# Kernel optimization log

Hardware: AMD Instinct MI355X
Metric: run time of the kernel (lower is better)

Reference implementation:

```python
import jax, jax.numpy as jnp
import numpy as np

HEAD_DIM = 64
EPS = 1e-06


def yat_dense(x, kernel, bias):
    # YatDense (nmn): y = (x.W)^2 / (||x - w||^2 + eps) * alpha_scale + b
    dot = x @ kernel                                  # [..., F]
    x_sq = jnp.sum(x * x, axis=-1, keepdims=True)     # [..., 1]
    w_sq = jnp.sum(kernel * kernel, axis=0)           # [F]
    dist = x_sq + w_sq - 2.0 * dot                    # squared euclidean distance
    y = (dot * dot) / (dist + EPS)
    feats = kernel.shape[1]
    scale = np.sqrt(feats) / np.log1p(feats)          # alpha=1 scaling
    return y * jnp.asarray(scale, x.dtype) + bias


def apply_rope(q, k):
    # q,k: [B,H,T,D]; interleaved-pair rotation, base 10000 (dim=HEAD_DIM)
    B, H, T, D = q.shape
    half = D // 2
    pos = jnp.arange(T, dtype=jnp.float32)
    freqs = 10000.0 ** (-jnp.arange(half, dtype=jnp.float32) / half)
    ang = pos[:, None] * freqs[None, :]               # [T, half]
    sin = jnp.sin(ang)[None, None, :, :, None]        # [1,1,T,half,1]
    cos = jnp.cos(ang)[None, None, :, :, None]

    def rot(t):
        ts = t.reshape(B, H, T, half, 2)
        t0, t1 = ts[..., 0:1], ts[..., 1:2]
        out = jnp.concatenate([t0 * cos - t1 * sin, t1 * cos + t0 * sin], axis=-1)
        return out.reshape(B, H, T, D)

    return rot(q), rot(k)


def setup_inputs() -> dict:
    key = jax.random.key(0)
    B, T, C, H = 2, 2048, 1024, 16
    k1, k2, k3, k4, k5 = jax.random.split(key, 5)
    x = jax.random.normal(k1, (B, T, C), dtype=jnp.float32)
    # causal mask, broadcast over batch
    mask = jnp.broadcast_to(jnp.tril(jnp.ones((T, T), dtype=bool))[None], (B, T, T))
    s = 1.0 / np.sqrt(C)
    w_attn = jax.random.normal(k2, (C, 3 * C), dtype=jnp.float32) * s
    b_attn = jnp.zeros((3 * C,), dtype=jnp.float32)
    w_proj = jax.random.normal(k3, (C, C), dtype=jnp.float32) * s
    b_proj = jnp.zeros((C,), dtype=jnp.float32)
    return {"x": x, "mask": mask, "w_attn": w_attn, "b_attn": b_attn,
            "w_proj": w_proj, "b_proj": b_proj}


def reference(x, mask, w_attn, b_attn, w_proj, b_proj):
    B, T, C = x.shape
    H = C // HEAD_DIM
    qkv = yat_dense(x, w_attn, b_attn)                     # [B,T,3C]
    qkv = qkv.reshape(B, T, 3, H, HEAD_DIM)
    q, k, v = jnp.moveaxis(qkv, 2, 0)                      # each [B,T,H,hd]
    q = jnp.swapaxes(q, 1, 2)                              # [B,H,T,hd]
    k = jnp.swapaxes(k, 1, 2)
    v = jnp.swapaxes(v, 1, 2)
    q, k = apply_rope(q, k)
    scale = jnp.asarray(np.sqrt(HEAD_DIM), x.dtype)
    attn = jnp.einsum('bhqd,bhkd->bhqk', q, k) / scale     # [B,H,T,T]
    neg = jnp.finfo(x.dtype).min
    attn = jnp.where(mask[:, None, :, :], attn, neg)
    attn = jax.nn.softmax(attn, axis=-1)
    out = jnp.einsum('bhqk,bhkd->bhqd', attn, v)           # [B,H,T,hd]
    out = jnp.swapaxes(out, 1, 2).reshape(B, T, C)
    return yat_dense(out, w_proj, b_proj)
```

## Files before the change

kernel.cpp:

```cpp
#include <hip/hip_runtime.h>
#include <hip/hip_bf16.h>
#include <cmath>

#define BB 2
#define TT 2048
#define CC 1024
#define HH 16
#define DD 64
#define ROWS (BB*TT)
#define N1 (3*CC)
#define EPS 1e-6f

using short8 = __attribute__((ext_vector_type(8))) short;
using f32x4  = __attribute__((ext_vector_type(4))) float;

__device__ __forceinline__ void gl_lds16(const __hip_bfloat16* g, unsigned short* l) {
    __builtin_amdgcn_global_load_lds(
        (const __attribute__((address_space(1))) unsigned int*)(g),
        (__attribute__((address_space(3))) unsigned int*)(l), 16, 0, 0);
}

__device__ __forceinline__ unsigned int bf16pair(float a, float b) {
    __hip_bfloat16 ha = (__hip_bfloat16)a, hb = (__hip_bfloat16)b;
    unsigned short ua = *(unsigned short*)&ha, ub = *(unsigned short*)&hb;
    return (unsigned int)ua | ((unsigned int)ub << 16);
}

__device__ __forceinline__ float bf2f(unsigned short u) {
    unsigned int v = (unsigned int)u << 16;
    return *(float*)&v;
}

__global__ void aux_rowsq(const float* __restrict__ X, float* __restrict__ xsq,
                          __hip_bfloat16* __restrict__ Xb, float* __restrict__ osq,
                          float* __restrict__ rope,
                          float* __restrict__ wsqa, float* __restrict__ wsqp) {
    int blk = blockIdx.x;
    int t = threadIdx.x;
    if (blk >= ROWS) {
        int idx = (blk - ROWS) * 256 + t;
        if (idx < N1) wsqa[idx] = 0.f;
        if (idx < CC) wsqp[idx] = 0.f;
        if (idx < TT * 32) {
            int tt = idx >> 5, i = idx & 31;
            double freq = pow(10000.0, -(double)i / 32.0);
            float ang = (float)tt * (float)freq;
            rope[idx * 2 + 0] = cosf(ang);
            rope[idx * 2 + 1] = sinf(ang);
        }
        return;
    }
    int row = blk;
    const float* xr = X + (size_t)row * CC;
    __hip_bfloat16* br = Xb + (size_t)row * CC;
    float p = 0.f;
#pragma unroll
    for (int i = 0; i < 4; ++i) {
        float v = xr[t + i * 256];
        p += v * v;
        br[t + i * 256] = (__hip_bfloat16)v;
    }
#pragma unroll
    for (int off = 32; off > 0; off >>= 1) p += __shfl_xor(p, off, 64);
    __shared__ float s4[4];
    if ((t & 63) == 0) s4[t >> 6] = p;
    __syncthreads();
    if (t == 0) { xsq[row] = s4[0] + s4[1] + s4[2] + s4[3]; osq[row] = 0.f; }
}

__global__ void transpose2(const float* __restrict__ Wa, __hip_bfloat16* __restrict__ WaT,
                           float* __restrict__ wsqa,
                           const float* __restrict__ Wp, __hip_bfloat16* __restrict__ WpT,
                           float* __restrict__ wsqp) {
    const float* W; __hip_bfloat16* Wt; float* wsq; int N;
    if (blockIdx.z == 0) { W = Wa; Wt = WaT; wsq = wsqa; N = N1; }
    else { if (blockIdx.x >= 16) return; W = Wp; Wt = WpT; wsq = wsqp; N = CC; }
    const int K = CC;
    __shared__ unsigned short tile[64][65];
    int n0 = blockIdx.x * 64, k0 = blockIdx.y * 64;
    int c = threadIdx.x & 63, rg = threadIdx.x >> 6;
    float part = 0.f;
#pragma unroll
    for (int rr = 0; rr < 16; ++rr) {
        int r = rg + rr * 4;
        float f = W[(size_t)(k0 + r) * N + n0 + c];
        __hip_bfloat16 h = (__hip_bfloat16)f;
        tile[r][c] = *(unsigned short*)&h;
        part += f * f;
    }
    atomicAdd(&wsq[n0 + c], part);
    __syncthreads();
#pragma unroll
    for (int rr = 0; rr < 16; ++rr) {
        int r = rg + rr * 4;
        unsigned short u = tile[c][r];
        Wt[(size_t)(n0 + r) * K + k0 + c] = *(__hip_bfloat16*)&u;
    }
}

__global__ __launch_bounds__(256) void yat_gemm_qkv2(
    const __hip_bfloat16* __restrict__ A,
    const __hip_bfloat16* __restrict__ Bt,
    const float* __restrict__ xsq, const float* __restrict__ wsq,
    const float* __restrict__ bias,
    __hip_bfloat16* __restrict__ Qb, __hip_bfloat16* __restrict__ Kb,
    __hip_bfloat16* __restrict__ Vb, float scale) {
    const int K = CC;
    __shared__ __align__(16) unsigned short As0[128 * 32], As1[128 * 32];
    __shared__ __align__(16) unsigned short Bs0[128 * 32], Bs1[128 * 32];
    int tid = threadIdx.x;
    int wave = tid >> 6, lane = tid & 63, quad = lane >> 4, l16 = lane & 15;
    int wr = wave >> 1, wc = wave & 1;
    int m0 = blockIdx.y * 128, n0 = blockIdx.x * 128;

    f32x4 acc[4][4];
#pragma unroll
    for (int mt = 0; mt < 4; ++mt)
#pragma unroll
        for (int nt = 0; nt < 4; ++nt) acc[mt][nt] = f32x4{0.f, 0.f, 0.f, 0.f};

    int srow = lane >> 2, soff = (lane & 3) << 3;
    for (int k0 = 0; k0 < K; k0 += 64) {
        __syncthreads();
#pragma unroll
        for (int i = 0; i < 2; ++i) {
            int rowc = (wave * 2 + i) * 16;
            const __hip_bfloat16* ap = A + (size_t)(m0 + rowc + srow) * K + k0 + soff;
            gl_lds16(ap,      As0 + rowc * 32);
            gl_lds16(ap + 32, As1 + rowc * 32);
            const __hip_bfloat16* bp = Bt + (size_t)(n0 + rowc + srow) * K + k0 + soff;
            gl_lds16(bp,      Bs0 + rowc * 32);
            gl_lds16(bp + 32, Bs1 + rowc * 32);
        }
        __syncthreads();
#pragma unroll
        for (int h = 0; h < 2; ++h) {
            const unsigned short* Ah = h ? As1 : As0;
            const unsigned short* Bh = h ? Bs1 : Bs0;
            short8 af[4], bf[4];
#pragma unroll
            for (int mt = 0; mt < 4; ++mt)
                af[mt] = *(const short8*)(Ah + (wr * 64 + mt * 16 + l16) * 32 + quad * 8);
#pragma unroll
            for (int nt = 0; nt < 4; ++nt)
                bf[nt] = *(const short8*)(Bh + (wc * 64 + nt * 16 + l16) * 32 + quad * 8);
#pragma unroll
            for (int mt = 0; mt < 4; ++mt)
#pragma unroll
                for (int nt = 0; nt < 4; ++nt)
                    acc[mt][nt] = __builtin_amdgcn_mfma_f32_16x16x32_bf16(af[mt], bf[nt], acc[mt][nt], 0, 0, 0);
        }
    }
    int mb = m0 + wr * 64 + quad * 4;
#pragma unroll
    for (int nt = 0; nt < 4; ++nt) {
        int col = n0 + wc * 64 + nt * 16 + l16;
        float wq = wsq[col], bs = bias[col];
        int sec = col >> 10, cc2 = col & 1023;
        int h = cc2 >> 6, d = cc2 & 63;
        __hip_bfloat16* dst = (sec == 0) ? Qb : ((sec == 1) ? Kb : Vb);
#pragma unroll
        for (int mt = 0; mt < 4; ++mt) {
#pragma unroll
            for (int r = 0; r < 4; ++r) {
                int row = mb + mt * 16 + r;
                float dot = acc[mt][nt][r];
                float dist = xsq[row] + wq - 2.f * dot + EPS;
                float y = dot * dot / dist * scale + bs;
                int t = row & (TT - 1), bI = row >> 11;
                dst[(((size_t)bI * HH + h) * TT + t) * DD + d] = (__hip_bfloat16)y;
            }
        }
    }
}

__global__ __launch_bounds__(256) void ropek_vtrans(
    unsigned short* __restrict__ Kb, const unsigned short* __restrict__ Vb,
    __hip_bfloat16* __restrict__ Vtb, const float* __restrict__ rope) {
    int bh = blockIdx.y, t0 = blockIdx.x * 64, tid = threadIdx.x;
    __shared__ unsigned short vt[64][72];
    int r = tid >> 2, g = tid & 3;
    const unsigned short* src = Vb + ((size_t)bh * TT + t0 + r) * DD + g * 16;
    *(uint4*)&vt[r][g * 16]     = *(const uint4*)src;
    *(uint4*)&vt[r][g * 16 + 8] = *(const uint4*)(src + 8);
    {
        int t = t0 + r;
        unsigned short* kp = Kb + ((size_t)bh * TT + t) * DD + g * 16;
        union U8 { uint4 v; unsigned short s[8]; } k0v, k1v, o0, o1;
        k0v.v = *(const uint4*)kp;
        k1v.v = *(const uint4*)(kp + 8);
        const float* rp = rope + (size_t)t * 64 + g * 16;
#pragma unroll
        for (int u = 0; u < 8; ++u) {
            float c = rp[2 * u], sn = rp[2 * u + 1];
            unsigned short ev = (u < 4) ? k0v.s[2 * u]     : k1v.s[2 * u - 8];
            unsigned short ov = (u < 4) ? k0v.s[2 * u + 1] : k1v.s[2 * u - 7];
            float f0 = bf2f(ev), f1 = bf2f(ov);
            unsigned int pr = bf16pair(f0 * c - f1 * sn, f1 * c + f0 * sn);
            if (u < 4) ((unsigned int*)&o0)[u] = pr;
            else       ((unsigned int*)&o1)[u - 4] = pr;
        }
        *(uint4*)kp = o0.v;
        *(uint4*)(kp + 8) = o1.v;
    }
    __syncthreads();
    union U8b { uint4 v; unsigned short s[8]; };
#pragma unroll
    for (int p = 0; p < 2; ++p) {
        int d = (tid >> 3) + p * 32, tl = (tid & 7) * 8;
        U8b w;
#pragma unroll
        for (int j = 0; j < 8; ++j) w.s[j] = vt[tl + j][d];
        *(uint4*)(Vtb + ((size_t)bh * DD + d) * TT + t0 + tl) = w.v;
    }
}

__global__ __launch_bounds__(256, 4) void attn_mfma10(
    const __hip_bfloat16* __restrict__ Qb, const __hip_bfloat16* __restrict__ Kb,
    const __hip_bfloat16* __restrict__ Vtb, const float* __restrict__ rope,
    __hip_bfloat16* __restrict__ out, float* __restrict__ osq) {
    const float QSC = 0.125f * 1.44269504f;
    int i = blockIdx.x;
    int xcd = i & 7;
    int r0 = i >> 3;
    int bh = xcd + 8 * (r0 & 3);
    int rr = r0 >> 2;
    int v = rr & 7, s2 = rr >> 3;
    int qblk = (s2 == 0) ? v : (s2 == 1) ? (15 - v) : (s2 == 2) ? (16 + v) : (31 - v);
    int b = bh >> 4, h = bh & 15;
    int tid = threadIdx.x;
    int wave = tid >> 6, lane = tid & 63, quad = lane >> 4, l16 = lane & 15;

    __shared__ __align__(16) unsigned short Ks[2][2][64 * 32];
    __shared__ __align__(16) unsigned short Vs[2][2][64 * 32];
    __shared__ __align__(16) unsigned short Ps[4][16 * 64];
    unsigned short* pp = &Ps[wave][0];
    int sw = l16 & 7;

    const __hip_bfloat16* Qbase = Qb + (size_t)bh * TT * DD;
    const __hip_bfloat16* Kbase = Kb + (size_t)bh * TT * DD;
    const __hip_bfloat16* Vbase = Vtb + (size_t)bh * DD * TT;

    int qw = qblk * 64 + wave * 16;
    short8 qf0, qf1;
    {
        int t = qw + l16;
        const unsigned short* qr = (const unsigned short*)(Qbase + (size_t)t * DD) + quad * 8;
        union S8 { short8 v; unsigned short s[8]; } r0v, r1v, o0v, o1v;
        r0v.v = *(const short8*)qr;
        r1v.v = *(const short8*)(qr + 32);
        const float* rpa = rope + (size_t)t * 64 + quad * 8;
        const float* rpb = rpa + 32;
#pragma unroll
        for (int u = 0; u < 4; ++u) {
            float c = rpa[2 * u] * QSC, sn = rpa[2 * u + 1] * QSC;
            float e = bf2f(r0v.s[2 * u]), o = bf2f(r0v.s[2 * u + 1]);
            ((unsigned int*)&o0v)[u] = bf16pair(e * c - o * sn, o * c + e * sn);
            float c2 = rpb[2 * u] * QSC, sn2 = rpb[2 * u + 1] * QSC;
            float e2 = bf2f(r1v.s[2 * u]), o2 = bf2f(r1v.s[2 * u + 1]);
            ((unsigned int*)&o1v)[u] = bf16pair(e2 * c2 - o2 * sn2, o2 * c2 + e2 * sn2);
        }
        qf0 = o0v.v;
        qf1 = o1v.v;
    }
    short8 ones8;
#pragma unroll
    for (int u = 0; u < 8; ++u) ones8[u] = (short)0x3F80;

    f32x4 acc_o[4];
#pragma unroll
    for (int mt = 0; mt < 4; ++mt) acc_o[mt] = f32x4{0.f, 0.f, 0.f, 0.f};
    f32x4 acc_l = {0.f, 0.f, 0.f, 0.f};

    int srow = lane >> 2, soff = (lane & 3) * 8;
    int q_g = qw + l16;

    gl_lds16(Kbase + (size_t)(wave * 16 + srow) * DD + soff,      &Ks[0][0][wave * 512]);
    gl_lds16(Kbase + (size_t)(wave * 16 + srow) * DD + 32 + soff, &Ks[0][1][wave * 512]);
    gl_lds16(Vbase + (size_t)(wave * 16 + srow) * TT + soff,      &Vs[0][0][wave * 512]);
    gl_lds16(Vbase + (size_t)(wave * 16 + srow) * TT + 32 + soff, &Vs[0][1][wave * 512]);

    for (int kt = 0; kt <= qblk; ++kt) {
        int cur = kt & 1;
        int k0 = kt * 64;
        __syncthreads();
        if (kt < qblk) {
            int nb = cur ^ 1, kn = k0 + 64;
            gl_lds16(Kbase + (size_t)(kn + wave * 16 + srow) * DD + soff,      &Ks[nb][0][wave * 512]);
            gl_lds16(Kbase + (size_t)(kn + wave * 16 + srow) * DD + 32 + soff, &Ks[nb][1][wave * 512]);
            gl_lds16(Vbase + (size_t)(wave * 16 + srow) * TT + kn + soff,      &Vs[nb][0][wave * 512]);
            gl_lds16(Vbase + (size_t)(wave * 16 + srow) * TT + kn + 32 + soff, &Vs[nb][1][wave * 512]);
        }
        f32x4 accs[4];
#pragma unroll
        for (int mt = 0; mt < 4; ++mt) {
            short8 kf0 = *(const short8*)(&Ks[cur][0][(mt * 16 + l16) * 32 + quad * 8]);
            short8 kf1 = *(const short8*)(&Ks[cur][1][(mt * 16 + l16) * 32 + quad * 8]);
            f32x4 z = {0.f, 0.f, 0.f, 0.f};
            z = __builtin_amdgcn_mfma_f32_16x16x32_bf16(kf0, qf0, z, 0, 0, 0);
            accs[mt] = __builtin_amdgcn_mfma_f32_16x16x32_bf16(kf1, qf1, z, 0, 0, 0);
        }
        int limit = (kt == qblk) ? q_g : 0x7FFFFFFF;
#pragma unroll
        for (int mt = 0; mt < 4; ++mt) {
            int keyb = k0 + mt * 16 + quad * 4;
            float p0 = exp2f(accs[mt][0]);
            float p1 = exp2f(accs[mt][1]);
            float p2 = exp2f(accs[mt][2]);
            float p3 = exp2f(accs[mt][3]);
            p0 = (keyb + 0 <= limit) ? p0 : 0.f;
            p1 = (keyb + 1 <= limit) ? p1 : 0.f;
            p2 = (keyb + 2 <= limit) ? p2 : 0.f;
            p3 = (keyb + 3 <= limit) ? p3 : 0.f;
            uint2 w2;
            w2.x = bf16pair(p0, p1);
            w2.y = bf16pair(p2, p3);
            int off = (((mt * 2 + (quad >> 1)) ^ sw) << 3) + ((quad & 1) << 2);
            *(uint2*)(pp + (l16 << 6) + off) = w2;
        }
        short8 pf0 = *(const short8*)(pp + (l16 << 6) + ((quad ^ sw) << 3));
        short8 pf1 = *(const short8*)(pp + (l16 << 6) + (((4 + quad) ^ sw) << 3));
#pragma unroll
        for (int mt = 0; mt < 4; ++mt) {
            short8 vf0 = *(const short8*)(&Vs[cur][0][(mt * 16 + l16) * 32 + quad * 8]);
            short8 vf1 = *(const short8*)(&Vs[cur][1][(mt * 16 + l16) * 32 + quad * 8]);
            acc_o[mt] = __builtin_amdgcn_mfma_f32_16x16x32_bf16(vf0, pf0, acc_o[mt], 0, 0, 0);
            acc_o[mt] = __builtin_amdgcn_mfma_f32_16x16x32_bf16(vf1, pf1, acc_o[mt], 0, 0, 0);
        }
        acc_l = __builtin_amdgcn_mfma_f32_16x16x32_bf16(ones8, pf0, acc_l, 0, 0, 0);
        acc_l = __builtin_amdgcn_mfma_f32_16x16x32_bf16(ones8, pf1, acc_l, 0, 0, 0);
    }
    float inv = 1.f / acc_l[0];
    float part = 0.f;
#pragma unroll
    for (int mt = 0; mt < 4; ++mt) {
        float o0 = acc_o[mt][0] * inv;
        float o1 = acc_o[mt][1] * inv;
        float o2 = acc_o[mt][2] * inv;
        float o3 = acc_o[mt][3] * inv;
        part += o0 * o0 + o1 * o1 + o2 * o2 + o3 * o3;
        uint2 w2;
        w2.x = bf16pair(o0, o1);
        w2.y = bf16pair(o2, o3);
        int off = (((mt * 2 + (quad >> 1)) ^ sw) << 3) + ((quad & 1) << 2);
        *(uint2*)(pp + (l16 << 6) + off) = w2;
    }
    part += __shfl_xor(part, 16, 64);
    part += __shfl_xor(part, 32, 64);
    if (quad == 0) atomicAdd(&osq[(size_t)b * TT + qw + l16], part);
    int rw = lane >> 2, cg = lane & 3, sw2 = rw & 7;
    uint4 o0 = *(const uint4*)(pp + (rw << 6) + (((cg * 2) ^ sw2) << 3));
    uint4 o1 = *(const uint4*)(pp + (rw << 6) + (((cg * 2 + 1) ^ sw2) << 3));
    __hip_bfloat16* orow = out + (size_t)(b * TT + qw + rw) * CC + h * DD + cg * 16;
    *(uint4*)(orow) = o0;
    *(uint4*)(orow + 8) = o1;
}

template<int TM, int TN, typename OutT>
__global__ __launch_bounds__(256) void yat_gemm_bk64(
    const __hip_bfloat16* __restrict__ A,
    const __hip_bfloat16* __restrict__ Bt,
    const float* __restrict__ xsq, const float* __restrict__ wsq,
    const float* __restrict__ bias, OutT* __restrict__ C,
    int M, int N, int K, float scale) {
    constexpr int MT = TM / 32;
    constexpr int NT = TN / 32;
    constexpr int IA = TM / 64;
    constexpr int IB = TN / 64;
    __shared__ __align__(16) unsigned short As0[TM * 32];
    __shared__ __align__(16) unsigned short As1[TM * 32];
    __shared__ __align__(16) unsigned short Bs0[TN * 32];
    __shared__ __align__(16) unsigned short Bs1[TN * 32];
    int tid = threadIdx.x;
    int wave = tid >> 6, lane = tid & 63, quad = lane >> 4, l16 = lane & 15;
    int wr = wave >> 1, wc = wave & 1;
    int m0 = blockIdx.y * TM, n0 = blockIdx.x * TN;

    f32x4 acc[MT][NT];
#pragma unroll
    for (int mt = 0; mt < MT; ++mt)
#pragma unroll
        for (int nt = 0; nt < NT; ++nt) acc[mt][nt] = f32x4{0.f, 0.f, 0.f, 0.f};

    int srow = lane >> 2, soff = (lane & 3) << 3;
    for (int k0 = 0; k0 < K; k0 += 64) {
        __syncthreads();
#pragma unroll
        for (int i = 0; i < IA; ++i) {
            int rowc = (wave * IA + i) * 16;
            const __hip_bfloat16* ap = A + (size_t)(m0 + rowc + srow) * K + k0 + soff;
            gl_lds16(ap,      As0 + rowc * 32);
            gl_lds16(ap + 32, As1 + rowc * 32);
        }
#pragma unroll
        for (int i = 0; i < IB; ++i) {
            int rowc = (wave * IB + i) * 16;
            const __hip_bfloat16* bp = Bt + (size_t)(n0 + rowc + srow) * K + k0 + soff;
            gl_lds16(bp,      Bs0 + rowc * 32);
            gl_lds16(bp + 32, Bs1 + rowc * 32);
        }
        __syncthreads();
#pragma unroll
        for (int h = 0; h < 2; ++h) {
            const unsigned short* Ah = h ? As1 : As0;
            const unsigned short* Bh = h ? Bs1 : Bs0;
            short8 af[MT], bf[NT];
#pragma unroll
            for (int mt = 0; mt < MT; ++mt)
                af[mt] = *(const short8*)(Ah + (wr * (TM / 2) + mt * 16 + l16) * 32 + quad * 8);
#pragma unroll
            for (int nt = 0; nt < NT; ++nt)
                bf[nt] = *(const short8*)(Bh + (wc * (TN / 2) + nt * 16 + l16) * 32 + quad * 8);
#pragma unroll
            for (int mt = 0; mt < MT; ++mt)
#pragma unroll
                for (int nt = 0; nt < NT; ++nt)
                    acc[mt][nt] = __builtin_amdgcn_mfma_f32_16x16x32_bf16(af[mt], bf[nt], acc[mt][nt], 0, 0, 0);
        }
    }
    int mb = m0 + wr * (TM / 2) + quad * 4;
#pragma unroll
    for (int nt = 0; nt < NT; ++nt) {
        int col = n0 + wc * (TN / 2) + nt * 16 + l16;
        float wq = wsq[col];
        float bs = bias[col];
#pragma unroll
        for (int mt = 0; mt < MT; ++mt) {
#pragma unroll
            for (int r = 0; r < 4; ++r) {
                int row = mb + mt * 16 + r;
                float dot = acc[mt][nt][r];
                float dist = xsq[row] + wq - 2.f * dot + EPS;
                C[(size_t)row * N + col] = (OutT)(dot * dot / dist * scale + bs);
            }
        }
    }
}

extern "C" void kernel_launch(void* const* d_in, const int* in_sizes, int n_in,
                              void* d_out, int out_size, void* d_ws, size_t ws_size,
                              hipStream_t stream) {
    const float* x      = (const float*)d_in[0];
    const float* w_attn = (const float*)d_in[2];
    const float* b_attn = (const float*)d_in[3];
    const float* w_proj = (const float*)d_in[4];
    const float* b_proj = (const float*)d_in[5];
    float* out = (float*)d_out;

    char* ws = (char*)d_ws;
    __hip_bfloat16* xbf  = (__hip_bfloat16*)(ws + 0);
    __hip_bfloat16* aout = (__hip_bfloat16*)(ws + 8388608);
    __hip_bfloat16* watT = (__hip_bfloat16*)(ws + 16777216);
    __hip_bfloat16* wpT  = (__hip_bfloat16*)(ws + 23068672);
    float*          rope = (float*)(ws + 25165824);
    float*          xsq  = (float*)(ws + 25690112);
    float*          osq  = (float*)(ws + 25706496);
    float*          wsqa = (float*)(ws + 25722880);
    float*          wsqp = (float*)(ws + 25735168);
    __hip_bfloat16* Qb   = (__hip_bfloat16*)(ws + 25739264);
    __hip_bfloat16* Kb   = (__hip_bfloat16*)(ws + 34127872);
    __hip_bfloat16* Vb   = (__hip_bfloat16*)(ws + 42516480);
    __hip_bfloat16* Vtb  = (__hip_bfloat16*)(ws + 50905088);

    float scale1 = (float)(sqrt(3072.0) / log1p(3072.0));
    float scale2 = (float)(sqrt(1024.0) / log1p(1024.0));

    aux_rowsq<<<ROWS + 256, 256, 0, stream>>>(x, xsq, xbf, osq, rope, wsqa, wsqp);
    transpose2<<<dim3(48, 16, 2), 256, 0, stream>>>(w_attn, watT, wsqa, w_proj, wpT, wsqp);
    yat_gemm_qkv2<<<dim3(N1 / 128, ROWS / 128), 256, 0, stream>>>(
        xbf, watT, xsq, wsqa, b_attn, Qb, Kb, Vb, scale1);
    ropek_vtrans<<<dim3(TT / 64, BB * HH), 256, 0, stream>>>(
        (unsigned short*)Kb, (const unsigned short*)Vb, Vtb, rope);
    attn_mfma10<<<1024, 256, 0, stream>>>(Qb, Kb, Vtb, rope, aout, osq);
    yat_gemm_bk64<64, 64, float><<<dim3(CC / 64, ROWS / 64), 256, 0, stream>>>(
        aout, wpT, osq, wsqp, b_proj, out, ROWS, CC, CC, scale2);
}
```

Before: 222.0 us.

## Merge prep kernels, write V transposed from QKV GEMM epilogue

Merges row-norm/bf16 conversion, rope table and weight transpose into one launch, where each block loops over all K tiles and reduces its column norms without atomics. The QKV GEMM epilogue now writes V directly in transposed layout, so the separate V transpose pass and the intermediate V buffer go away, leaving a slimmer RoPE-only kernel for K. The intent is to cut launches and extra memory traffic. In exchange, only 64 blocks now do the serialized weight-transpose work, which could become a long tail.

```diff
diff --git a/kernel.cpp b/kernel.cpp
--- a/kernel.cpp
+++ b/kernel.cpp
@@ -31,80 +31,79 @@
     return *(float*)&v;
 }
 
-__global__ void aux_rowsq(const float* __restrict__ X, float* __restrict__ xsq,
+__global__ void prep_all2(const float* __restrict__ X, float* __restrict__ xsq,
                           __hip_bfloat16* __restrict__ Xb, float* __restrict__ osq,
                           float* __restrict__ rope,
-                          float* __restrict__ wsqa, float* __restrict__ wsqp) {
+                          const float* __restrict__ Wa, __hip_bfloat16* __restrict__ WaT,
+                          float* __restrict__ wsqa,
+                          const float* __restrict__ Wp, __hip_bfloat16* __restrict__ WpT,
+                          float* __restrict__ wsqp) {
     int blk = blockIdx.x;
     int t = threadIdx.x;
-    if (blk >= ROWS) {
-        int idx = (blk - ROWS) * 256 + t;
-        if (idx < N1) wsqa[idx] = 0.f;
-        if (idx < CC) wsqp[idx] = 0.f;
-        if (idx < TT * 32) {
-            int tt = idx >> 5, i = idx & 31;
-            double freq = pow(10000.0, -(double)i / 32.0);
-            float ang = (float)tt * (float)freq;
-            rope[idx * 2 + 0] = cosf(ang);
-            rope[idx * 2 + 1] = sinf(ang);
-        }
+    if (blk < 64) {
+        const float* W; __hip_bfloat16* Wt; float* wsq; int N, n0;
+        if (blk < 48) { W = Wa; Wt = WaT; wsq = wsqa; N = N1; n0 = blk * 64; }
+        else          { W = Wp; Wt = WpT; wsq = wsqp; N = CC; n0 = (blk - 48) * 64; }
+        __shared__ unsigned short tile[64][65];
+        __shared__ float sred[4][64];
+        int c = t & 63, rg = t >> 6;
+        float part = 0.f;
+        for (int kt = 0; kt < 16; ++kt) {
+            int k0 = kt * 64;
+            __syncthreads();
+#pragma unroll
+            for (int rr = 0; rr < 16; ++rr) {
+                int r = rg + rr * 4;
+                float f = W[(size_t)(k0 + r) * N + n0 + c];
+                __hip_bfloat16 hh = (__hip_bfloat16)f;
+                tile[r][c] = *(unsigned short*)&hh;
+                part += f * f;
+            }
+            __syncthreads();
+#pragma unroll
+            for (int rr = 0; rr < 16; ++rr) {
+                int r = rg + rr * 4;
+                unsigned short u = tile[c][r];
+                Wt[(size_t)(n0 + r) * CC + k0 + c] = *(__hip_bfloat16*)&u;
+            }
+        }
+        sred[rg][c] = part;
+        __syncthreads();
+        if (rg == 0) wsq[n0 + c] = sred[0][c] + sred[1][c] + sred[2][c] + sred[3][c];
         return;
     }
-    int row = blk;
-    const float* xr = X + (size_t)row * CC;
-    __hip_bfloat16* br = Xb + (size_t)row * CC;
-    float p = 0.f;
-#pragma unroll
-    for (int i = 0; i < 4; ++i) {
-        float v = xr[t + i * 256];
-        p += v * v;
-        br[t + i * 256] = (__hip_bfloat16)v;
-    }
-#pragma unroll
-    for (int off = 32; off > 0; off >>= 1) p += __shfl_xor(p, off, 64);
-    __shared__ float s4[4];
-    if ((t & 63) == 0) s4[t >> 6] = p;
-    __syncthreads();
-    if (t == 0) { xsq[row] = s4[0] + s4[1] + s4[2] + s4[3]; osq[row] = 0.f; }
-}
-
-__global__ void transpose2(const float* __restrict__ Wa, __hip_bfloat16* __restrict__ WaT,
-                           float* __restrict__ wsqa,
-                           const float* __restrict__ Wp, __hip_bfloat16* __restrict__ WpT,
-                           float* __restrict__ wsqp) {
-    const float* W; __hip_bfloat16* Wt; float* wsq; int N;
-    if (blockIdx.z == 0) { W = Wa; Wt = WaT; wsq = wsqa; N = N1; }
-    else { if (blockIdx.x >= 16) return; W = Wp; Wt = WpT; wsq = wsqp; N = CC; }
-    const int K = CC;
-    __shared__ unsigned short tile[64][65];
-    int n0 = blockIdx.x * 64, k0 = blockIdx.y * 64;
-    int c = threadIdx.x & 63, rg = threadIdx.x >> 6;
-    float part = 0.f;
-#pragma unroll
-    for (int rr = 0; rr < 16; ++rr) {
-        int r = rg + rr * 4;
-        float f = W[(size_t)(k0 + r) * N + n0 + c];
-        __hip_bfloat16 h = (__hip_bfloat16)f;
-        tile[r][c] = *(unsigned short*)&h;
-        part += f * f;
-    }
-    atomicAdd(&wsq[n0 + c], part);
-    __syncthreads();
-#pragma unroll
-    for (int rr = 0; rr < 16; ++rr) {
-        int r = rg + rr * 4;
-        unsigned short u = tile[c][r];
-        Wt[(size_t)(n0 + r) * K + k0 + c] = *(__hip_bfloat16*)&u;
-    }
-}
-
-__global__ __launch_bounds__(256) void yat_gemm_qkv2(
+    if (blk < 64 + ROWS) {
+        int row = blk - 64;
+        const float* xr = X + (size_t)row * CC + t * 4;
+        float4 v = *(const float4*)xr;
+        float p = v.x * v.x + v.y * v.y + v.z * v.z + v.w * v.w;
+        uint2 w;
+        w.x = bf16pair(v.x, v.y);
+        w.y = bf16pair(v.z, v.w);
+        *(uint2*)((unsigned short*)Xb + (size_t)row * CC + t * 4) = w;
+#pragma unroll
+        for (int off = 32; off > 0; off >>= 1) p += __shfl_xor(p, off, 64);
+        __shared__ float s4[4];
+        if ((t & 63) == 0) s4[t >> 6] = p;
+        __syncthreads();
+        if (t == 0) { xsq[row] = s4[0] + s4[1] + s4[2] + s4[3]; osq[row] = 0.f; }
+        return;
+    }
+    int idx = (blk - 64 - ROWS) * 256 + t;
+    int tt = idx >> 5, i = idx & 31;
+    double freq = pow(10000.0, -(double)i / 32.0);
+    float ang = (float)tt * (float)freq;
+    rope[idx * 2 + 0] = cosf(ang);
+    rope[idx * 2 + 1] = sinf(ang);
+}
+
+__global__ __launch_bounds__(256) void yat_gemm_qkv3(
     const __hip_bfloat16* __restrict__ A,
     const __hip_bfloat16* __restrict__ Bt,
     const float* __restrict__ xsq, const float* __restrict__ wsq,
     const float* __restrict__ bias,
     __hip_bfloat16* __restrict__ Qb, __hip_bfloat16* __restrict__ Kb,
-    __hip_bfloat16* __restrict__ Vb, float scale) {
+    __hip_bfloat16* __restrict__ Vtb, float scale) {
     const int K = CC;
     __shared__ __align__(16) unsigned short As0[128 * 32], As1[128 * 32];
     __shared__ __align__(16) unsigned short Bs0[128 * 32], Bs1[128 * 32];
@@ -152,67 +151,74 @@
         }
     }
     int mb = m0 + wr * 64 + quad * 4;
-#pragma unroll
-    for (int nt = 0; nt < 4; ++nt) {
-        int col = n0 + wc * 64 + nt * 16 + l16;
-        float wq = wsq[col], bs = bias[col];
-        int sec = col >> 10, cc2 = col & 1023;
-        int h = cc2 >> 6, d = cc2 & 63;
-        __hip_bfloat16* dst = (sec == 0) ? Qb : ((sec == 1) ? Kb : Vb);
-#pragma unroll
-        for (int mt = 0; mt < 4; ++mt) {
-#pragma unroll
-            for (int r = 0; r < 4; ++r) {
-                int row = mb + mt * 16 + r;
-                float dot = acc[mt][nt][r];
-                float dist = xsq[row] + wq - 2.f * dot + EPS;
-                float y = dot * dot / dist * scale + bs;
-                int t = row & (TT - 1), bI = row >> 11;
-                dst[(((size_t)bI * HH + h) * TT + t) * DD + d] = (__hip_bfloat16)y;
+    int sec = n0 >> 10;
+    if (sec == 2) {
+#pragma unroll
+        for (int nt = 0; nt < 4; ++nt) {
+            int col = n0 + wc * 64 + nt * 16 + l16;
+            float wq = wsq[col], bs = bias[col];
+            int cc2 = col & 1023, h = cc2 >> 6, d = cc2 & 63;
+#pragma unroll
+            for (int mt = 0; mt < 4; ++mt) {
+                int rowb = mb + mt * 16;
+                int bI = rowb >> 11, tb2 = rowb & (TT - 1);
+                float y[4];
+#pragma unroll
+                for (int r = 0; r < 4; ++r) {
+                    float dot = acc[mt][nt][r];
+                    float dist = xsq[rowb + r] + wq - 2.f * dot + EPS;
+                    y[r] = dot * dot / dist * scale + bs;
+                }
+                uint2 w2;
+                w2.x = bf16pair(y[0], y[1]);
+                w2.y = bf16pair(y[2], y[3]);
+                *(uint2*)((unsigned short*)Vtb + (((size_t)bI * HH + h) * DD + d) * TT + tb2) = w2;
             }
         }
-    }
-}
-
-__global__ __launch_bounds__(256) void ropek_vtrans(
-    unsigned short* __restrict__ Kb, const unsigned short* __restrict__ Vb,
-    __hip_bfloat16* __restrict__ Vtb, const float* __restrict__ rope) {
-    int bh = blockIdx.y, t0 = blockIdx.x * 64, tid = threadIdx.x;
-    __shared__ unsigned short vt[64][72];
-    int r = tid >> 2, g = tid & 3;
-    const unsigned short* src = Vb + ((size_t)bh * TT + t0 + r) * DD + g * 16;
-    *(uint4*)&vt[r][g * 16]     = *(const uint4*)src;
-    *(uint4*)&vt[r][g * 16 + 8] = *(const uint4*)(src + 8);
-    {
-        int t = t0 + r;
-        unsigned short* kp = Kb + ((size_t)bh * TT + t) * DD + g * 16;
-        union U8 { uint4 v; unsigned short s[8]; } k0v, k1v, o0, o1;
-        k0v.v = *(const uint4*)kp;
-        k1v.v = *(const uint4*)(kp + 8);
-        const float* rp = rope + (size_t)t * 64 + g * 16;
-#pragma unroll
-        for (int u = 0; u < 8; ++u) {
-            float c = rp[2 * u], sn = rp[2 * u + 1];
-            unsigned short ev = (u < 4) ? k0v.s[2 * u]     : k1v.s[2 * u - 8];
-            unsigned short ov = (u < 4) ? k0v.s[2 * u + 1] : k1v.s[2 * u - 7];
-            float f0 = bf2f(ev), f1 = bf2f(ov);
-            unsigned int pr = bf16pair(f0 * c - f1 * sn, f1 * c + f0 * sn);
-            if (u < 4) ((unsigned int*)&o0)[u] = pr;
-            else       ((unsigned int*)&o1)[u - 4] = pr;
-        }
-        *(uint4*)kp = o0.v;
-        *(uint4*)(kp + 8) = o1.v;
-    }
-    __syncthreads();
-    union U8b { uint4 v; unsigned short s[8]; };
-#pragma unroll
-    for (int p = 0; p < 2; ++p) {
-        int d = (tid >> 3) + p * 32, tl = (tid & 7) * 8;
-        U8b w;
-#pragma unroll
-        for (int j = 0; j < 8; ++j) w.s[j] = vt[tl + j][d];
-        *(uint4*)(Vtb + ((size_t)bh * DD + d) * TT + t0 + tl) = w.v;
-    }
+    } else {
+        __hip_bfloat16* dst = sec ? Kb : Qb;
+#pragma unroll
+        for (int nt = 0; nt < 4; ++nt) {
+            int col = n0 + wc * 64 + nt * 16 + l16;
+            float wq = wsq[col], bs = bias[col];
+            int cc2 = col & 1023, h = cc2 >> 6, d = cc2 & 63;
+#pragma unroll
+            for (int mt = 0; mt < 4; ++mt) {
+#pragma unroll
+                for (int r = 0; r < 4; ++r) {
+                    int row = mb + mt * 16 + r;
+                    float dot = acc[mt][nt][r];
+                    float dist = xsq[row] + wq - 2.f * dot + EPS;
+                    float yv = dot * dot / dist * scale + bs;
+                    int t2 = row & (TT - 1), bI = row >> 11;
+                    dst[(((size_t)bI * HH + h) * TT + t2) * DD + d] = (__hip_bfloat16)yv;
+                }
+            }
+        }
+    }
+}
+
+__global__ __launch_bounds__(256) void ropek(
+    unsigned short* __restrict__ Kb, const float* __restrict__ rope) {
+    int u = blockIdx.x * 256 + threadIdx.x;
+    int bh = u >> 13, r2 = u & 8191, t = r2 >> 2, g = r2 & 3;
+    unsigned short* kp = Kb + (((size_t)bh * TT) + t) * DD + g * 16;
+    union U8 { uint4 v; unsigned short s[8]; } k0v, k1v, o0, o1;
+    k0v.v = *(const uint4*)kp;
+    k1v.v = *(const uint4*)(kp + 8);
+    const float* rp = rope + (size_t)t * 64 + g * 16;
+#pragma unroll
+    for (int uu = 0; uu < 8; ++uu) {
+        float c = rp[2 * uu], sn = rp[2 * uu + 1];
+        unsigned short ev = (uu < 4) ? k0v.s[2 * uu]     : k1v.s[2 * uu - 8];
+        unsigned short ov = (uu < 4) ? k0v.s[2 * uu + 1] : k1v.s[2 * uu - 7];
+        float f0 = bf2f(ev), f1 = bf2f(ov);
+        unsigned int pr = bf16pair(f0 * c - f1 * sn, f1 * c + f0 * sn);
+        if (uu < 4) ((unsigned int*)&o0)[uu] = pr;
+        else        ((unsigned int*)&o1)[uu - 4] = pr;
+    }
+    *(uint4*)kp = o0.v;
+    *(uint4*)(kp + 8) = o1.v;
 }
 
 __global__ __launch_bounds__(256, 4) void attn_mfma10(
@@ -459,18 +465,16 @@
     float*          wsqp = (float*)(ws + 25735168);
     __hip_bfloat16* Qb   = (__hip_bfloat16*)(ws + 25739264);
     __hip_bfloat16* Kb   = (__hip_bfloat16*)(ws + 34127872);
-    __hip_bfloat16* Vb   = (__hip_bfloat16*)(ws + 42516480);
-    __hip_bfloat16* Vtb  = (__hip_bfloat16*)(ws + 50905088);
+    __hip_bfloat16* Vtb  = (__hip_bfloat16*)(ws + 42516480);
 
     float scale1 = (float)(sqrt(3072.0) / log1p(3072.0));
     float scale2 = (float)(sqrt(1024.0) / log1p(1024.0));
 
-    aux_rowsq<<<ROWS + 256, 256, 0, stream>>>(x, xsq, xbf, osq, rope, wsqa, wsqp);
-    transpose2<<<dim3(48, 16, 2), 256, 0, stream>>>(w_attn, watT, wsqa, w_proj, wpT, wsqp);
-    yat_gemm_qkv2<<<dim3(N1 / 128, ROWS / 128), 256, 0, stream>>>(
-        xbf, watT, xsq, wsqa, b_attn, Qb, Kb, Vb, scale1);
-    ropek_vtrans<<<dim3(TT / 64, BB * HH), 256, 0, stream>>>(
-        (unsigned short*)Kb, (const unsigned short*)Vb, Vtb, rope);
+    prep_all2<<<64 + ROWS + 256, 256, 0, stream>>>(
+        x, xsq, xbf, osq, rope, w_attn, watT, wsqa, w_proj, wpT, wsqp);
+    yat_gemm_qkv3<<<dim3(N1 / 128, ROWS / 128), 256, 0, stream>>>(
+        xbf, watT, xsq, wsqa, b_attn, Qb, Kb, Vtb, scale1);
+    ropek<<<1024, 256, 0, stream>>>((unsigned short*)Kb, rope);
     attn_mfma10<<<1024, 256, 0, stream>>>(Qb, Kb, Vtb, rope, aout, osq);
     yat_gemm_bk64<64, 64, float><<<dim3(CC / 64, ROWS / 64), 256, 0, stream>>>(
         aout, wpT, osq, wsqp, b_proj, out, ROWS, CC, CC, scale2);
```

Measured after the change: 239.8 us. 1.08x slower.
